# Kernel optimization log

Measured on AMD Instinct MI355X. Metric: run time of the kernel, lower is better.

The kernel has to match this reference:

```python
import jax, jax.numpy as jnp
import numpy as np

SEQ, WORD, EMBED, NHEAD = 2048, 1024, 128, 16


def setup_inputs() -> dict:
    key = jax.random.key(0)
    ks = jax.random.split(key, 6)
    sw = 1.0 / np.sqrt(WORD)  # xavier-ish scale for linear weights
    sp = 1.0 / np.sqrt(EMBED * NHEAD)
    return {
        "x": jax.random.normal(ks[0], (SEQ, WORD), jnp.float32),
        "Wq": jax.random.normal(ks[1], (NHEAD, WORD, EMBED), jnp.float32) * sw,
        "bq": jnp.zeros((NHEAD, EMBED), jnp.float32),
        "Wk": jax.random.normal(ks[2], (NHEAD, WORD, EMBED), jnp.float32) * sw,
        "bk": jnp.zeros((NHEAD, EMBED), jnp.float32),
        "Wv": jax.random.normal(ks[3], (NHEAD, WORD, EMBED), jnp.float32) * sw,
        "bv": jnp.zeros((NHEAD, EMBED), jnp.float32),
        "proj": jax.random.normal(ks[4], (NHEAD * EMBED, EMBED), jnp.float32) * sp,
    }


def reference(x, Wq, bq, Wk, bk, Wv, bv, proj):
    # Batched-head equivalent of the per-head Attention ModuleList loop.
    # x: [S, W]; Wq/Wk/Wv: [H, W, E]; b*: [H, E]; proj: [H*E, E]
    Q = jnp.einsum("sw,hwe->hse", x, Wq) + bq[:, None, :]
    K = jnp.einsum("sw,hwe->hse", x, Wk) + bk[:, None, :]
    V = jnp.einsum("sw,hwe->hse", x, Wv) + bv[:, None, :]
    scale = 1.0 / jnp.sqrt(jnp.asarray(EMBED, x.dtype))
    scores = jnp.einsum("hqe,hke->hqk", Q, K) * scale  # [H, S, S]
    attn = jax.nn.softmax(scores, axis=-1)
    Z = jnp.einsum("hqk,hke->hqe", attn, V)  # [H, S, E]
    # torch.cat([...], dim=1): per-head outputs side-by-side -> [S, H*E]
    Z_s = jnp.transpose(Z, (1, 0, 2)).reshape(x.shape[0], -1)
    return Z_s @ proj  # [S, E]
```

## Files before the change

### kernel.cpp

```cpp
#include <hip/hip_runtime.h>
#include <stdint.h>

#define GAS __attribute__((address_space(1)))
#define LAS __attribute__((address_space(3)))

typedef unsigned short u16;
typedef __attribute__((ext_vector_type(8))) __bf16 bf16x8;
typedef __attribute__((ext_vector_type(4))) float f32x4;

#define SEQ 2048
#define WORD 1024
#define EMBED 128
#define NHEAD 16

__device__ __forceinline__ u16 f2b(float f) {
  return __builtin_bit_cast(u16, (__bf16)f);
}

__global__ __launch_bounds__(256) void cast_x_kernel(const float* __restrict__ x,
                                                     u16* __restrict__ xb) {
  int i = (blockIdx.x * 256 + threadIdx.x) * 4;
  float4 v = *(const float4*)(x + i);
  ushort4 o;
  o.x = f2b(v.x); o.y = f2b(v.y); o.z = f2b(v.z); o.w = f2b(v.w);
  *(ushort4*)(xb + i) = o;
}

__global__ __launch_bounds__(256) void transpose_cast_kernel(
    const float* __restrict__ s0, const float* __restrict__ s1,
    const float* __restrict__ s2, u16* __restrict__ d0, u16* __restrict__ d1,
    u16* __restrict__ d2, int R, int C, long stride, int zsel) {
  __shared__ float tile[32][33];
  const float* s;
  u16* d;
  if (zsel) {
    int z = blockIdx.z;
    int wsel = z >> 4, hh = z & 15;
    s = (wsel == 0 ? s0 : wsel == 1 ? s1 : s2) + (long)hh * stride;
    d = (wsel == 0 ? d0 : wsel == 1 ? d1 : d2) + (long)hh * stride;
  } else {
    s = s0; d = d0;
  }
  int r0 = blockIdx.x * 32, c0 = blockIdx.y * 32;
  int tx = threadIdx.x & 31, ty = threadIdx.x >> 5;
#pragma unroll
  for (int i = 0; i < 4; ++i)
    tile[ty + i * 8][tx] = s[(long)(r0 + ty + i * 8) * C + c0 + tx];
  __syncthreads();
#pragma unroll
  for (int i = 0; i < 4; ++i)
    d[(long)(c0 + ty + i * 8) * R + r0 + tx] = f2b(tile[tx][ty + i * 8]);
}

template <typename OUT>
__device__ __forceinline__ void gemm128(const u16* __restrict__ A, const u16* __restrict__ B,
                                        OUT* __restrict__ C, int lda, int ldb, int ldc,
                                        int ksteps, const float* biasN, const float* biasM,
                                        float scale) {
  __shared__ u16 lA[128 * 64];
  __shared__ u16 lB[128 * 64];
  const int tid = threadIdx.x;
  const int l = tid & 63, w = tid >> 6;
  const int quad = l >> 4, ln = l & 15;
  const int wm = w >> 1, wn = w & 1;
  f32x4 acc[4][4] = {};
  for (int ks = 0; ks < ksteps; ++ks) {
    const u16* Ak = A + ks * 64;
    const u16* Bk = B + ks * 64;
    __syncthreads();
#pragma unroll
    for (int i = 0; i < 4; ++i) {
      int idx = w * 256 + i * 64 + l;
      int r = idx >> 3, cp = idx & 7;
      int cg = cp ^ (r & 7);
      __builtin_amdgcn_global_load_lds((const GAS void*)(Ak + (long)r * lda + cg * 8),
                                       (LAS void*)(lA + (w * 256 + i * 64) * 8), 16, 0, 0);
      __builtin_amdgcn_global_load_lds((const GAS void*)(Bk + (long)r * ldb + cg * 8),
                                       (LAS void*)(lB + (w * 256 + i * 64) * 8), 16, 0, 0);
    }
    __syncthreads();
    bf16x8 af[2][4], bfv[2][4];
#pragma unroll
    for (int kc = 0; kc < 2; ++kc) {
#pragma unroll
      for (int i = 0; i < 4; ++i) {
        int c = kc * 4 + quad;
        int rm = wm * 64 + i * 16 + ln;
        af[kc][i] = *(const bf16x8*)(lA + rm * 64 + ((c ^ (rm & 7)) * 8));
        int rn = wn * 64 + i * 16 + ln;
        bfv[kc][i] = *(const bf16x8*)(lB + rn * 64 + ((c ^ (rn & 7)) * 8));
      }
    }
#pragma unroll
    for (int kc = 0; kc < 2; ++kc)
#pragma unroll
      for (int i = 0; i < 4; ++i)
#pragma unroll
        for (int j = 0; j < 4; ++j)
          acc[i][j] = __builtin_amdgcn_mfma_f32_16x16x32_bf16(af[kc][i], bfv[kc][j],
                                                              acc[i][j], 0, 0, 0);
  }
#pragma unroll
  for (int i = 0; i < 4; ++i) {
#pragma unroll
    for (int j = 0; j < 4; ++j) {
      int row0 = wm * 64 + i * 16 + quad * 4;
      int col = wn * 64 + j * 16 + ln;
      float bn = biasN ? biasN[col] : 0.f;
#pragma unroll
      for (int reg = 0; reg < 4; ++reg) {
        int row = row0 + reg;
        float bm = biasM ? biasM[row] : 0.f;
        float v = (acc[i][j][reg] + bn + bm) * scale;
        if constexpr (sizeof(OUT) == 2)
          C[(long)row * ldc + col] = (OUT)f2b(v);
        else
          C[(long)row * ldc + col] = v;
      }
    }
  }
}

__global__ __launch_bounds__(256, 3) void qkv_gemm_kernel(
    const u16* __restrict__ xb, const u16* __restrict__ Wqt, const u16* __restrict__ Wkt,
    const u16* __restrict__ Wvt, const float* __restrict__ bq, const float* __restrict__ bk,
    const float* __restrict__ bv, u16* __restrict__ Q, u16* __restrict__ Kb,
    u16* __restrict__ Vt) {
  const int t = blockIdx.x;
  const int h = blockIdx.y;
  const int which = blockIdx.z;
  const float qscale = 0.12753042123789493f;
  if (which == 0) {
    gemm128<u16>(xb + t * 128 * WORD, Wqt + h * EMBED * WORD,
                 Q + h * SEQ * EMBED + t * 128 * EMBED, WORD, WORD, EMBED,
                 WORD / 64, bq + h * EMBED, nullptr, qscale);
  } else if (which == 1) {
    gemm128<u16>(xb + t * 128 * WORD, Wkt + h * EMBED * WORD,
                 Kb + h * SEQ * EMBED + t * 128 * EMBED, WORD, WORD, EMBED,
                 WORD / 64, bk + h * EMBED, nullptr, 1.f);
  } else {
    gemm128<u16>(Wvt + h * EMBED * WORD, xb + t * 128 * WORD,
                 Vt + h * EMBED * SEQ + t * 128, WORD, WORD, SEQ,
                 WORD / 64, nullptr, bv + h * EMBED, 1.f);
  }
}

__global__ __launch_bounds__(256, 2) void attn_kernel(const u16* __restrict__ Q,
                                                      const u16* __restrict__ K,
                                                      const u16* __restrict__ V,
                                                      u16* __restrict__ Zs) {
  __shared__ u16 lKV[4 * 8192];
  __shared__ u16 lP[4 * 16 * 72];
  const int h = blockIdx.y, qb = blockIdx.x;
  const int tid = threadIdx.x;
  const int l = tid & 63, w = tid >> 6, quad = l >> 4, ln = l & 15;
  const int wr = w >> 1, wk = w & 1;
  const u16* Qh = Q + h * SEQ * EMBED;
  const u16* Kh = K + h * SEQ * EMBED;
  const u16* Vh = V + h * EMBED * SEQ;
  u16* Pw = lP + w * (16 * 72);
  const int q0 = qb * 64 + wr * 32;
  const u16* myK = lKV + wk * 8192;
  const u16* myV = lKV + 16384 + wk * 8192;

  bf16x8 qf[2][4];
#pragma unroll
  for (int rs = 0; rs < 2; ++rs)
#pragma unroll
    for (int kc = 0; kc < 4; ++kc)
      qf[rs][kc] = *(const bf16x8*)(Qh + (q0 + rs * 16 + ln) * EMBED + kc * 32 + quad * 8);

  const __bf16 ov = (ln == 0) ? (__bf16)1.0f : (__bf16)0.0f;
  const bf16x8 onesf = {ov, ov, ov, ov, ov, ov, ov, ov};

  f32x4 oacc[2][8] = {};
  f32x4 lacc[2] = {};

  for (int sup = 0; sup < SEQ / 128; ++sup) {
    __syncthreads();
#pragma unroll
    for (int j = 0; j < 8; ++j) {
      int kb = j >> 2;
      int cb = (j & 3) * 256 + w * 64;
      int c = cb + l;
      int rk = c >> 4, cgk = (c & 15) ^ (rk & 15);
      __builtin_amdgcn_global_load_lds(
          (const GAS void*)(Kh + (sup * 128 + kb * 64 + rk) * EMBED + cgk * 8),
          (LAS void*)(lKV + kb * 8192 + cb * 8), 16, 0, 0);
      int rv = c >> 3, cgv = (c & 7) ^ (rv & 7);
      __builtin_amdgcn_global_load_lds(
          (const GAS void*)(Vh + rv * SEQ + sup * 128 + kb * 64 + cgv * 8),
          (LAS void*)(lKV + 16384 + kb * 8192 + cb * 8), 16, 0, 0);
    }
    __syncthreads();
    f32x4 sacc[2][4] = {};
#pragma unroll
    for (int kc = 0; kc < 4; ++kc) {
      bf16x8 kf[4];
#pragma unroll
      for (int ns = 0; ns < 4; ++ns) {
        int kr = ns * 16 + ln;
        kf[ns] = *(const bf16x8*)(myK + kr * 128 + (((kc * 4 + quad) ^ (kr & 15)) * 8));
      }
#pragma unroll
      for (int ns = 0; ns < 4; ++ns)
#pragma unroll
        for (int rs = 0; rs < 2; ++rs)
          sacc[rs][ns] = __builtin_amdgcn_mfma_f32_16x16x32_bf16(qf[rs][kc], kf[ns],
                                                                 sacc[rs][ns], 0, 0, 0);
    }
    bf16x8 vf[2][8];
#pragma unroll
    for (int kc = 0; kc < 2; ++kc)
#pragma unroll
      for (int es = 0; es < 8; ++es) {
        int er = es * 16 + ln;
        vf[kc][es] = *(const bf16x8*)(myV + er * 64 + (((kc * 4 + quad) ^ (er & 7)) * 8));
      }
#pragma unroll
    for (int rs = 0; rs < 2; ++rs) {
#pragma unroll
      for (int ns = 0; ns < 4; ++ns)
#pragma unroll
        for (int r = 0; r < 4; ++r)
          Pw[(quad * 4 + r) * 72 + ns * 16 + ln] = f2b(exp2f(sacc[rs][ns][r]));
#pragma unroll
      for (int kc = 0; kc < 2; ++kc) {
        bf16x8 pa = *(const bf16x8*)(Pw + ln * 72 + kc * 32 + quad * 8);
#pragma unroll
        for (int es = 0; es < 8; ++es)
          oacc[rs][es] = __builtin_amdgcn_mfma_f32_16x16x32_bf16(pa, vf[kc][es],
                                                                 oacc[rs][es], 0, 0, 0);
        lacc[rs] = __builtin_amdgcn_mfma_f32_16x16x32_bf16(pa, onesf, lacc[rs], 0, 0, 0);
      }
    }
  }
  __syncthreads();
  float* lO = (float*)lKV;
  if (wk == 1) {
#pragma unroll
    for (int rs = 0; rs < 2; ++rs) {
#pragma unroll
      for (int es = 0; es < 8; ++es)
#pragma unroll
        for (int r = 0; r < 4; ++r)
          lO[wr * 4224 + (rs * 16 + quad * 4 + r) * 132 + es * 16 + ln] = oacc[rs][es][r];
      if (ln == 0)
#pragma unroll
        for (int r = 0; r < 4; ++r)
          lO[wr * 4224 + (rs * 16 + quad * 4 + r) * 132 + 128] = lacc[rs][r];
    }
  }
  __syncthreads();
  if (wk == 0) {
#pragma unroll
    for (int rs = 0; rs < 2; ++rs)
#pragma unroll
      for (int r = 0; r < 4; ++r) {
        int lrow = rs * 16 + quad * 4 + r;
        float lsum = __shfl(lacc[rs][r], l & 48) + lO[wr * 4224 + lrow * 132 + 128];
        float rl = 1.f / lsum;
        int srow = q0 + lrow;
#pragma unroll
        for (int es = 0; es < 8; ++es) {
          float o = oacc[rs][es][r] + lO[wr * 4224 + lrow * 132 + es * 16 + ln];
          Zs[(long)srow * (NHEAD * EMBED) + h * EMBED + es * 16 + ln] = f2b(o * rl);
        }
      }
  }
}

__global__ __launch_bounds__(256, 2) void final_gemm_kernel(const u16* __restrict__ Zs,
                                                            const u16* __restrict__ projT,
                                                            float* __restrict__ pbuf) {
  const int t = blockIdx.x;
  const int kc = blockIdx.y;
  gemm128<float>(Zs + (long)t * 128 * (NHEAD * EMBED) + kc * 256, projT + kc * 256,
                 pbuf + (long)kc * SEQ * EMBED + t * 128 * EMBED,
                 NHEAD * EMBED, NHEAD * EMBED, EMBED, 4, nullptr, nullptr, 1.f);
}

__global__ __launch_bounds__(256) void reduce_kernel(const float* __restrict__ pbuf,
                                                     float* __restrict__ out) {
  int i = (blockIdx.x * 256 + threadIdx.x) * 4;
  float4 s = {0.f, 0.f, 0.f, 0.f};
#pragma unroll
  for (int kc = 0; kc < 8; ++kc) {
    float4 v = *(const float4*)(pbuf + (long)kc * SEQ * EMBED + i);
    s.x += v.x; s.y += v.y; s.z += v.z; s.w += v.w;
  }
  *(float4*)(out + i) = s;
}

extern "C" void kernel_launch(void* const* d_in, const int* in_sizes, int n_in,
                              void* d_out, int out_size, void* d_ws, size_t ws_size,
                              hipStream_t stream) {
  const float* x    = (const float*)d_in[0];
  const float* Wq   = (const float*)d_in[1];
  const float* bq   = (const float*)d_in[2];
  const float* Wk   = (const float*)d_in[3];
  const float* bk   = (const float*)d_in[4];
  const float* Wv   = (const float*)d_in[5];
  const float* bv   = (const float*)d_in[6];
  const float* proj = (const float*)d_in[7];
  float* out = (float*)d_out;

  char* ws = (char*)d_ws;
  u16* xb    = (u16*)(ws);
  u16* Wqt   = (u16*)(ws + (4L << 20));
  u16* Wkt   = (u16*)(ws + (8L << 20));
  u16* Wvt   = (u16*)(ws + (12L << 20));
  u16* projT = (u16*)(ws + (16L << 20));
  u16* Qm    = (u16*)(ws + (17L << 20));
  u16* Km    = (u16*)(ws + (26L << 20));
  u16* Vt    = (u16*)(ws + (35L << 20));
  u16* Zs    = (u16*)(ws + (44L << 20));
  float* pbuf = (float*)(ws);

  cast_x_kernel<<<dim3(SEQ * WORD / 1024), dim3(256), 0, stream>>>(x, xb);
  transpose_cast_kernel<<<dim3(WORD / 32, EMBED / 32, 48), dim3(256), 0, stream>>>(
      Wq, Wk, Wv, Wqt, Wkt, Wvt, WORD, EMBED, (long)WORD * EMBED, 1);
  transpose_cast_kernel<<<dim3(SEQ / 32, EMBED / 32, 1), dim3(256), 0, stream>>>(
      proj, nullptr, nullptr, projT, nullptr, nullptr, SEQ, EMBED, 0, 0);

  qkv_gemm_kernel<<<dim3(16, NHEAD, 3), dim3(256), 0, stream>>>(
      xb, Wqt, Wkt, Wvt, bq, bk, bv, Qm, Km, Vt);

  attn_kernel<<<dim3(32, NHEAD), dim3(256), 0, stream>>>(Qm, Km, Vt, Zs);

  final_gemm_kernel<<<dim3(16, 8), dim3(256), 0, stream>>>(Zs, projT, pbuf);
  reduce_kernel<<<dim3(SEQ * EMBED / 1024), dim3(256), 0, stream>>>(pbuf, out);
}
```

Baseline: 197.7 us.

## Double-buffer K/V tiles and enlarge attention query tile to 128 rows

Each attention block now handles 128 query rows instead of 64, so each wave holds four 16-row query subtiles. The K/V tile loads now prefetch the next 128-key tile into a second LDS buffer while the current one is computed, leaving one barrier per iteration. The V layout is changed to a single 128-wide swizzled tile. This aims to hide global-to-LDS latency and halve K/V reloads per query. In exchange LDS use roughly doubles and register pressure rises, limiting the kernel to one block (4 waves) per CU with half as many blocks, which reduces latency hiding through occupancy.

Result: slower. 212.3 us (+7.4%).

```diff
diff --git a/kernel.cpp b/kernel.cpp
--- a/kernel.cpp
+++ b/kernel.cpp
@@ -145,11 +145,11 @@
   }
 }
 
-__global__ __launch_bounds__(256, 2) void attn_kernel(const u16* __restrict__ Q,
+__global__ __launch_bounds__(256, 1) void attn_kernel(const u16* __restrict__ Q,
                                                       const u16* __restrict__ K,
                                                       const u16* __restrict__ V,
                                                       u16* __restrict__ Zs) {
-  __shared__ u16 lKV[4 * 8192];
+  __shared__ u16 lKV[2][2][16384];
   __shared__ u16 lP[4 * 16 * 72];
   const int h = blockIdx.y, qb = blockIdx.x;
   const int tid = threadIdx.x;
@@ -159,13 +159,11 @@
   const u16* Kh = K + h * SEQ * EMBED;
   const u16* Vh = V + h * EMBED * SEQ;
   u16* Pw = lP + w * (16 * 72);
-  const int q0 = qb * 64 + wr * 32;
-  const u16* myK = lKV + wk * 8192;
-  const u16* myV = lKV + 16384 + wk * 8192;
-
-  bf16x8 qf[2][4];
-#pragma unroll
-  for (int rs = 0; rs < 2; ++rs)
+  const int q0 = qb * 128 + wr * 64;
+
+  bf16x8 qf[4][4];
+#pragma unroll
+  for (int rs = 0; rs < 4; ++rs)
 #pragma unroll
     for (int kc = 0; kc < 4; ++kc)
       qf[rs][kc] = *(const bf16x8*)(Qh + (q0 + rs * 16 + ln) * EMBED + kc * 32 + quad * 8);
@@ -173,63 +171,69 @@
   const __bf16 ov = (ln == 0) ? (__bf16)1.0f : (__bf16)0.0f;
   const bf16x8 onesf = {ov, ov, ov, ov, ov, ov, ov, ov};
 
-  f32x4 oacc[2][8] = {};
-  f32x4 lacc[2] = {};
-
+  f32x4 oacc[4][8] = {};
+  f32x4 lacc[4] = {};
+
+  auto stage = [&](int sup, int buf) {
+#pragma unroll
+    for (int j = 0; j < 8; ++j) {
+      int cb = j * 256 + w * 64;
+      int c = cb + l;
+      int r = c >> 4, sc = c & 15, cg = sc ^ (r & 15);
+      __builtin_amdgcn_global_load_lds(
+          (const GAS void*)(Kh + (sup * 128 + r) * EMBED + cg * 8),
+          (LAS void*)(&lKV[buf][0][cb * 8]), 16, 0, 0);
+      __builtin_amdgcn_global_load_lds(
+          (const GAS void*)(Vh + r * SEQ + sup * 128 + cg * 8),
+          (LAS void*)(&lKV[buf][1][cb * 8]), 16, 0, 0);
+    }
+  };
+
+  stage(0, 0);
   for (int sup = 0; sup < SEQ / 128; ++sup) {
+    const int cur = sup & 1;
     __syncthreads();
-#pragma unroll
-    for (int j = 0; j < 8; ++j) {
-      int kb = j >> 2;
-      int cb = (j & 3) * 256 + w * 64;
-      int c = cb + l;
-      int rk = c >> 4, cgk = (c & 15) ^ (rk & 15);
-      __builtin_amdgcn_global_load_lds(
-          (const GAS void*)(Kh + (sup * 128 + kb * 64 + rk) * EMBED + cgk * 8),
-          (LAS void*)(lKV + kb * 8192 + cb * 8), 16, 0, 0);
-      int rv = c >> 3, cgv = (c & 7) ^ (rv & 7);
-      __builtin_amdgcn_global_load_lds(
-          (const GAS void*)(Vh + rv * SEQ + sup * 128 + kb * 64 + cgv * 8),
-          (LAS void*)(lKV + 16384 + kb * 8192 + cb * 8), 16, 0, 0);
-    }
-    __syncthreads();
-    f32x4 sacc[2][4] = {};
+    if (sup + 1 < SEQ / 128) stage(sup + 1, cur ^ 1);
+    const u16* Kb = lKV[cur][0];
+    const u16* Vb = lKV[cur][1];
+    f32x4 sacc[4][4] = {};
 #pragma unroll
     for (int kc = 0; kc < 4; ++kc) {
       bf16x8 kf[4];
 #pragma unroll
       for (int ns = 0; ns < 4; ++ns) {
-        int kr = ns * 16 + ln;
-        kf[ns] = *(const bf16x8*)(myK + kr * 128 + (((kc * 4 + quad) ^ (kr & 15)) * 8));
+        int kr = wk * 64 + ns * 16 + ln;
+        kf[ns] = *(const bf16x8*)(Kb + kr * 128 + (((kc * 4 + quad) ^ (kr & 15)) * 8));
       }
 #pragma unroll
       for (int ns = 0; ns < 4; ++ns)
 #pragma unroll
-        for (int rs = 0; rs < 2; ++rs)
+        for (int rs = 0; rs < 4; ++rs)
           sacc[rs][ns] = __builtin_amdgcn_mfma_f32_16x16x32_bf16(qf[rs][kc], kf[ns],
                                                                  sacc[rs][ns], 0, 0, 0);
     }
     bf16x8 vf[2][8];
 #pragma unroll
-    for (int kc = 0; kc < 2; ++kc)
+    for (int kc2 = 0; kc2 < 2; ++kc2)
 #pragma unroll
       for (int es = 0; es < 8; ++es) {
         int er = es * 16 + ln;
-        vf[kc][es] = *(const bf16x8*)(myV + er * 64 + (((kc * 4 + quad) ^ (er & 7)) * 8));
-      }
-#pragma unroll
-    for (int rs = 0; rs < 2; ++rs) {
+        vf[kc2][es] = *(const bf16x8*)(
+            Vb + er * 128 + (((wk * 8 + kc2 * 4 + quad) ^ (er & 15)) * 8));
+      }
+#pragma unroll
+    for (int rs = 0; rs < 4; ++rs) {
 #pragma unroll
       for (int ns = 0; ns < 4; ++ns)
 #pragma unroll
         for (int r = 0; r < 4; ++r)
           Pw[(quad * 4 + r) * 72 + ns * 16 + ln] = f2b(exp2f(sacc[rs][ns][r]));
 #pragma unroll
-      for (int kc = 0; kc < 2; ++kc) {
-        bf16x8 pa = *(const bf16x8*)(Pw + ln * 72 + kc * 32 + quad * 8);
+      for (int kc2 = 0; kc2 < 2; ++kc2) {
+        bf16x8 pa = *(const bf16x8*)(Pw + ln * 72 + kc2 * 32 + quad * 8);
 #pragma unroll
         for (int es = 0; es < 8; ++es)
-          oacc[rs][es] = __builtin_amdgcn_mfma_f32_16x16x32_bf16(pa, vf[kc][es],
+          oacc[rs][es] = __builtin_amdgcn_mfma_f32_16x16x32_bf16(pa, vf[kc2][es],
                                                                  oacc[rs][es], 0, 0, 0);
         lacc[rs] = __builtin_amdgcn_mfma_f32_16x16x32_bf16(pa, onesf, lacc[rs], 0, 0, 0);
       }
@@ -239,31 +243,31 @@
   float* lO = (float*)lKV;
   if (wk == 1) {
 #pragma unroll
-    for (int rs = 0; rs < 2; ++rs) {
+    for (int rs = 0; rs < 4; ++rs) {
 #pragma unroll
       for (int es = 0; es < 8; ++es)
 #pragma unroll
         for (int r = 0; r < 4; ++r)
-          lO[wr * 4224 + (rs * 16 + quad * 4 + r) * 132 + es * 16 + ln] = oacc[rs][es][r];
+          lO[(wr * 64 + rs * 16 + quad * 4 + r) * 132 + es * 16 + ln] = oacc[rs][es][r];
       if (ln == 0)
 #pragma unroll
         for (int r = 0; r < 4; ++r)
-          lO[wr * 4224 + (rs * 16 + quad * 4 + r) * 132 + 128] = lacc[rs][r];
+          lO[(wr * 64 + rs * 16 + quad * 4 + r) * 132 + 128] = lacc[rs][r];
     }
   }
   __syncthreads();
   if (wk == 0) {
 #pragma unroll
-    for (int rs = 0; rs < 2; ++rs)
+    for (int rs = 0; rs < 4; ++rs)
 #pragma unroll
       for (int r = 0; r < 4; ++r) {
-        int lrow = rs * 16 + quad * 4 + r;
-        float lsum = __shfl(lacc[rs][r], l & 48) + lO[wr * 4224 + lrow * 132 + 128];
+        int grow = wr * 64 + rs * 16 + quad * 4 + r;
+        float lsum = __shfl(lacc[rs][r], l & 48) + lO[grow * 132 + 128];
         float rl = 1.f / lsum;
-        int srow = q0 + lrow;
+        int srow = qb * 128 + grow;
 #pragma unroll
         for (int es = 0; es < 8; ++es) {
-          float o = oacc[rs][es][r] + lO[wr * 4224 + lrow * 132 + es * 16 + ln];
+          float o = oacc[rs][es][r] + lO[grow * 132 + es * 16 + ln];
           Zs[(long)srow * (NHEAD * EMBED) + h * EMBED + es * 16 + ln] = f2b(o * rl);
         }
       }
@@ -326,7 +330,7 @@
   qkv_gemm_kernel<<<dim3(16, NHEAD, 3), dim3(256), 0, stream>>>(
       xb, Wqt, Wkt, Wvt, bq, bk, bv, Qm, Km, Vt);
 
-  attn_kernel<<<dim3(32, NHEAD), dim3(256), 0, stream>>>(Qm, Km, Vt, Zs);
+  attn_kernel<<<dim3(16, NHEAD), dim3(256), 0, stream>>>(Qm, Km, Vt, Zs);
 
   final_gemm_kernel<<<dim3(16, 8), dim3(256), 0, stream>>>(Zs, projT, pbuf);
   reduce_kernel<<<dim3(SEQ * EMBED / 1024), dim3(256), 0, stream>>>(pbuf, out);
```
